# Performance work log

Hardware: AMD Instinct MI355X
Metric: run time of the kernel (lower is better)

The kernel has to match this reference:

```python
import jax, jax.numpy as jnp
import numpy as np

B, LTEXT, LVIS, D, H = 16, 128, 4096, 1024, 16
HD = D // H


def setup_inputs() -> dict:
    key = jax.random.key(0)
    ks = jax.random.split(key, 8)
    s = 0.02
    return {
        'hidden_states': jax.random.normal(ks[0], (B, LVIS, D), jnp.float32),
        'text_states': jax.random.normal(ks[1], (LTEXT, B, D), jnp.float32),
        'Wq': jax.random.normal(ks[2], (D, D), jnp.float32) * s,
        'bq': jnp.zeros((D,), jnp.float32),
        'Wk': jax.random.normal(ks[3], (D, D), jnp.float32) * s,
        'bk': jnp.zeros((D,), jnp.float32),
        'Wv': jax.random.normal(ks[4], (D, D), jnp.float32) * s,
        'bv': jnp.zeros((D,), jnp.float32),
        'Wo': jax.random.normal(ks[5], (D, D), jnp.float32) * s,
        'bo': jnp.zeros((D,), jnp.float32),
    }


def reference(hidden_states, text_states, Wq, bq, Wk, bk, Wv, bv, Wo, bo):
    # text_states: (L_text, B, D) -- code unpacks text_len, bsz from dims 0,1
    # hidden_states: (B, L_vis, D) -- key/value source
    Ltext, bsz, d = text_states.shape
    Lvis = hidden_states.shape[1]
    scale = HD ** -0.5

    # projections (torch Linear x @ W.T + b, here W stored already transposed)
    q = (text_states @ Wq + bq) * scale
    # faithful to torch .view: flatten memory then reshape to (B, Ltext, H, hd)
    q = q.reshape(bsz, Ltext, H, HD).transpose(0, 2, 1, 3)        # (B,H,Lt,hd)
    k = (hidden_states @ Wk + bk).reshape(bsz, Lvis, H, HD).transpose(0, 2, 1, 3)
    v = (hidden_states @ Wv + bv).reshape(bsz, Lvis, H, HD).transpose(0, 2, 1, 3)

    attn = jax.nn.softmax(jnp.einsum('bhtd,bhsd->bhts', q, k), axis=-1)  # (B,H,Lt,Lv)
    text_guided_vision = jnp.einsum('bhts,bhsd->bhtd', attn, v)          # (B,H,Lt,hd)
    # second matmul with transposed attention weights: P^T @ (P V)
    out = jnp.einsum('bhts,bhtd->bhsd', attn, text_guided_vision)        # (B,H,Lv,hd)

    out = out.transpose(0, 2, 1, 3).reshape(bsz, Lvis, d)
    return out @ Wo + bo
```

## Files before the change

### kernel.cpp

```cpp
#include <hip/hip_runtime.h>
#include <stdint.h>

typedef short  s16x8 __attribute__((ext_vector_type(8)));
typedef float  f32x4 __attribute__((ext_vector_type(4)));
typedef unsigned short u16x4 __attribute__((ext_vector_type(4)));

__device__ __forceinline__ unsigned short f2bf(float f) {
  unsigned u = __builtin_bit_cast(unsigned, f);
  u = (u + 0x7fffu + ((u >> 16) & 1u)) >> 16;
  return (unsigned short)u;
}

__device__ __forceinline__ void glds16(const void* g, void* l) {
  __builtin_amdgcn_global_load_lds((const __attribute__((address_space(1))) void*)g,
                                   (__attribute__((address_space(3))) void*)l, 16, 0, 0);
}

__device__ __forceinline__ f32x4 mfma16(s16x8 a, s16x8 b, f32x4 c) {
  return __builtin_amdgcn_mfma_f32_16x16x32_bf16(a, b, c, 0, 0, 0);
}

#define VM4 asm volatile("s_waitcnt vmcnt(4)" ::: "memory")
#define VM0 asm volatile("s_waitcnt vmcnt(0)" ::: "memory")

__global__ __launch_bounds__(256) void kt_cvt(const float* __restrict__ X,
                                              unsigned short* __restrict__ Y) {
  const size_t N8 = (size_t)16 * 4096 * 1024 / 8;
  for (size_t i = (size_t)blockIdx.x * 256 + threadIdx.x; i < N8;
       i += (size_t)gridDim.x * 256) {
    const float* g = X + i * 8;
    f32x4 a = *(const f32x4*)g;
    f32x4 b = *(const f32x4*)(g + 4);
    s16x8 o;
    o[0]=f2bf(a[0]); o[1]=f2bf(a[1]); o[2]=f2bf(a[2]); o[3]=f2bf(a[3]);
    o[4]=f2bf(b[0]); o[5]=f2bf(b[1]); o[6]=f2bf(b[2]); o[7]=f2bf(b[3]);
    *(s16x8*)(Y + i * 8) = o;
  }
}

__global__ void kt_transpose(const float* __restrict__ W, unsigned short* __restrict__ WT) {
  __shared__ float tile[64][65];
  int n0 = blockIdx.x * 64, k0 = blockIdx.y * 64;
  int tx = threadIdx.x, ty = threadIdx.y;
  #pragma unroll
  for (int r = ty; r < 64; r += 4)
    tile[r][tx] = W[(size_t)(k0 + r) * 1024 + n0 + tx];
  __syncthreads();
  #pragma unroll
  for (int r = ty; r < 64; r += 4)
    WT[(size_t)(n0 + r) * 1024 + k0 + tx] = f2bf(tile[tx][r]);
}

__global__ __launch_bounds__(256, 2) void kt_gemm_q(
    const float* __restrict__ Ain, const unsigned short* __restrict__ BT,
    const float* __restrict__ bias, unsigned short* __restrict__ Cout) {
  __shared__ __align__(16) unsigned short As[128 * 32];
  __shared__ __align__(16) unsigned short Bs[128 * 32];
  const int tid = threadIdx.x, lane = tid & 63, wave = tid >> 6;
  const int l15 = lane & 15, quad = lane >> 4;
  const int wr = wave >> 1, wc = wave & 1;
  const int n0 = blockIdx.x * 128, m0 = blockIdx.y * 128;

  f32x4 acc[4][4] = {};
  for (int k0 = 0; k0 < 1024; k0 += 32) {
    __syncthreads();
    #pragma unroll
    for (int i = 0; i < 2; ++i) {
      int rowb = (wave * 2 + i) * 16 + (lane >> 2);
      glds16(BT + (size_t)(n0 + rowb) * 1024 + k0 + (lane & 3) * 8,
             &Bs[(wave * 2 + i) * 512]);
    }
    {
      const float* A = Ain;
      int row = tid >> 1, ks = (tid & 1) * 16;
      const float* g = &A[(size_t)(m0 + row) * 1024 + k0 + ks];
      f32x4 fa = *(const f32x4*)(g);
      f32x4 fb = *(const f32x4*)(g + 4);
      f32x4 fc = *(const f32x4*)(g + 8);
      f32x4 fd = *(const f32x4*)(g + 12);
      s16x8 lo, hi;
      lo[0]=f2bf(fa[0]); lo[1]=f2bf(fa[1]); lo[2]=f2bf(fa[2]); lo[3]=f2bf(fa[3]);
      lo[4]=f2bf(fb[0]); lo[5]=f2bf(fb[1]); lo[6]=f2bf(fb[2]); lo[7]=f2bf(fb[3]);
      hi[0]=f2bf(fc[0]); hi[1]=f2bf(fc[1]); hi[2]=f2bf(fc[2]); hi[3]=f2bf(fc[3]);
      hi[4]=f2bf(fd[0]); hi[5]=f2bf(fd[1]); hi[6]=f2bf(fd[2]); hi[7]=f2bf(fd[3]);
      *(s16x8*)&As[row * 32 + ks] = lo;
      *(s16x8*)&As[row * 32 + ks + 8] = hi;
    }
    __syncthreads();
    s16x8 a[4], b[4];
    #pragma unroll
    for (int i = 0; i < 4; ++i) a[i] = *(const s16x8*)&As[(wr * 64 + i * 16 + l15) * 32 + quad * 8];
    #pragma unroll
    for (int j = 0; j < 4; ++j) b[j] = *(const s16x8*)&Bs[(wc * 64 + j * 16 + l15) * 32 + quad * 8];
    #pragma unroll
    for (int i = 0; i < 4; ++i)
      #pragma unroll
      for (int j = 0; j < 4; ++j) acc[i][j] = mfma16(a[i], b[j], acc[i][j]);
  }
  #pragma unroll
  for (int j = 0; j < 4; ++j) {
    int col = n0 + wc * 64 + j * 16 + l15;
    float bv = bias[col];
    #pragma unroll
    for (int i = 0; i < 4; ++i)
      #pragma unroll
      for (int r = 0; r < 4; ++r) {
        int row = m0 + wr * 64 + i * 16 + quad * 4 + r;
        float v = (acc[i][j][r] + bv) * 0.125f;
        size_t idx = ((size_t)((row >> 7) * 16 + (col >> 6)) * 128 + (row & 127)) * 64 + (col & 63);
        Cout[idx] = f2bf(v);
      }
  }
}

template <int MODE>
__global__ __launch_bounds__(512, 2) void kt_gemm256(
    const unsigned short* __restrict__ A, const unsigned short* __restrict__ BT,
    const float* __restrict__ bias0, const float* __restrict__ bias1,
    void* __restrict__ out0, void* __restrict__ out1) {
  constexpr int NN = (MODE == 0) ? 8 : 4;
  constexpr int CHUNK = (MODE == 0) ? 256 : 128;
  __shared__ __align__(16) unsigned short lds[65536];
  const int tid = threadIdx.x, lane = tid & 63, wave = tid >> 6;
  const int l15 = lane & 15, quad = lane >> 4;
  const int wr = wave >> 2, wc = wave & 3;
  const int r0 = lane >> 3, sck = (lane & 7) ^ r0;
  const int bid = blockIdx.x;
  const int logical = (bid & 7) * CHUNK + (bid >> 3);
  const int nblk = logical & (NN - 1), mblk = logical / NN;
  const int n0 = nblk * 256, m0 = mblk * 256;
  const unsigned short* Asrc = A + (size_t)m0 * 1024;
  const unsigned short* Bsrc = BT + (size_t)n0 * 1024;

  f32x4 acc[8][4] = {};
  s16x8 bf_[4][2];

  auto stageA = [&](int t, int h, int buf) {
    #pragma unroll
    for (int is = 0; is < 2; ++is) {
      int c = wave * 2 + is;
      glds16(Asrc + (size_t)(h * 128 + c * 8 + r0) * 1024 + t * 64 + sck * 8,
             &lds[buf * 32768 + h * 8192 + c * 512]);
    }
  };
  auto stageB = [&](int t, int h, int buf) {
    #pragma unroll
    for (int is = 0; is < 2; ++is) {
      int c = wave * 2 + is;
      glds16(Bsrc + (size_t)(h * 128 + c * 8 + r0) * 1024 + t * 64 + sck * 8,
             &lds[buf * 32768 + 16384 + h * 8192 + c * 512]);
    }
  };

  stageA(0, 0, 0); stageA(0, 1, 0); stageB(0, 0, 0); stageB(0, 1, 0);
  stageB(1, 0, 1); stageB(1, 1, 1);
  VM4;
  __builtin_amdgcn_s_barrier();

  #pragma unroll 1
  for (int it = 0; it < 8; ++it) {
    const bool last = (it == 7);
    const int te = 2 * it;
    #pragma unroll
    for (int half = 0; half < 2; ++half) {
      const int buf = half;
      #pragma unroll
      for (int p = 0; p < 4; ++p) {
        if (p == 0) {
          #pragma unroll
          for (int j = 0; j < 4; ++j)
            #pragma unroll
            for (int kk = 0; kk < 2; ++kk) {
              int r = (wc & 1) * 64 + j * 16 + l15;
              bf_[j][kk] = *(const s16x8*)&lds[buf * 32768 + 16384 + (wc >> 1) * 8192
                                               + r * 64 + (((kk * 4 + quad) ^ (r & 7)) << 3)];
            }
        }
        s16x8 af[2][2];
        #pragma unroll
        for (int ii = 0; ii < 2; ++ii)
          #pragma unroll
          for (int kk = 0; kk < 2; ++kk) {
            int r = (p * 2 + ii) * 16 + l15;
            af[ii][kk] = *(const s16x8*)&lds[buf * 32768 + wr * 8192
                                             + r * 64 + (((kk * 4 + quad) ^ (r & 7)) << 3)];
          }
        if (half == 0) {
          if (p == 0) { stageA(te + 1, 0, 1); stageA(te + 1, 1, 1); }
          else if (p == 1) { if (!last) stageB(te + 2, 0, 0); }
          else if (p == 2) { if (!last) stageB(te + 2, 1, 0); }
        } else {
          if (p == 0) { if (!last) stageA(te + 2, 0, 0); }
          else if (p == 1) { if (!last) { stageA(te + 2, 1, 0); stageB(te + 3, 0, 1); } }
          else if (p == 2) { if (!last) stageB(te + 3, 1, 1); }
        }
        __builtin_amdgcn_s_barrier();
        __builtin_amdgcn_s_setprio(1);
        #pragma unroll
        for (int ii = 0; ii < 2; ++ii)
          #pragma unroll
          for (int j = 0; j < 4; ++j)
            #pragma unroll
            for (int kk = 0; kk < 2; ++kk)
              acc[p * 2 + ii][j] = mfma16(af[ii][kk], bf_[j][kk], acc[p * 2 + ii][j]);
        __builtin_amdgcn_s_setprio(0);
        if (p == 3) {
          if (half == 0) { if (last) { VM0; } else { VM4; } }
          else           { if (!last) { VM4; } }
        }
        __builtin_amdgcn_s_barrier();
      }
    }
  }

  const int bb = m0 >> 12;
  const bool isV = (MODE == 0) && (n0 >= 1024);
  const float* bias = isV ? bias1 : bias0;
  #pragma unroll
  for (int j = 0; j < 4; ++j) {
    const int colg = n0 + wc * 64 + j * 16 + l15;
    const int c1 = colg & 1023;
    const float bv = bias[c1];
    const int hcol = c1 >> 6, dcol = c1 & 63;
    #pragma unroll
    for (int i = 0; i < 8; ++i) {
      const int row0 = m0 + wr * 128 + i * 16 + quad * 4;
      const int s = row0 & 4095;
      if constexpr (MODE == 0) {
        if (isV) {
          size_t base = (((size_t)bb * 16 + hcol) * 64 + dcol) * 4096 + s;
          u16x4 w;
          #pragma unroll
          for (int r = 0; r < 4; ++r) w[r] = f2bf(acc[i][j][r] + bv);
          *(u16x4*)&((unsigned short*)out1)[base] = w;
        } else {
          unsigned short* Ko = (unsigned short*)out0;
          size_t base = (((size_t)bb * 16 + hcol) * 4096 + s) * 64 + dcol;
          #pragma unroll
          for (int r = 0; r < 4; ++r) Ko[base + (size_t)r * 64] = f2bf(acc[i][j][r] + bv);
        }
      } else {
        float* O = (float*)out0;
        size_t base = (size_t)row0 * 1024 + colg;
        #pragma unroll
        for (int r = 0; r < 4; ++r) O[base + (size_t)r * 1024] = acc[i][j][r] + bv;
      }
    }
  }
}

__global__ __launch_bounds__(512, 4) void kt_attn1(
    const unsigned short* __restrict__ Qb, const unsigned short* __restrict__ Kb,
    const unsigned short* __restrict__ Vt, float* __restrict__ RpT,
    float* __restrict__ Zp) {
  __shared__ __align__(16) unsigned short Ks[2][128 * 64];
  __shared__ __align__(16) unsigned short Vts[2][64 * 128];
  __shared__ __align__(16) unsigned short Es[8][16 * 40];
  const int tid = threadIdx.x, lane = tid & 63, wave = tid >> 6;
  const int l15 = lane & 15, quad = lane >> 4;
  const int bid = blockIdx.x;
  const int lid = (bid & 7) * 128 + (bid >> 3);
  const int qidx = lid & 3, bh = lid >> 2;
  const size_t kbase = (size_t)bh * 4096 * 64;
  const size_t vbase = (size_t)bh * 64 * 4096;
  s16x8 qa[2];
  #pragma unroll
  for (int kk = 0; kk < 2; ++kk)
    qa[kk] = *(const s16x8*)&Qb[((size_t)bh * 128 + wave * 16 + l15) * 64 + kk * 32 + quad * 8];
  s16x8 bones;
  { unsigned short o = (l15 == 0) ? (unsigned short)0x3F80 : (unsigned short)0;
    #pragma unroll
    for (int c2 = 0; c2 < 8; ++c2) bones[c2] = (short)o; }
  f32x4 Racc[4] = {};
  f32x4 Zacc = {};

  auto stage = [&](int ch, int buf) {
    const int s0 = qidx * 1024 + ch * 128;
    #pragma unroll
    for (int i = 0; i < 2; ++i) {
      int srow = wave * 16 + i * 8 + (lane >> 3);
      int ck = (lane & 7) ^ (srow & 7);
      glds16(Kb + kbase + (size_t)(s0 + srow) * 64 + ck * 8,
             &Ks[buf][(wave * 16 + i * 8) * 64]);
    }
    #pragma unroll
    for (int i = 0; i < 2; ++i) {
      int drow = wave * 8 + i * 4 + (lane >> 4);
      int ck = (lane & 15) ^ (drow & 15);
      glds16(Vt + vbase + (size_t)drow * 4096 + s0 + ck * 8,
             &Vts[buf][(wave * 8 + i * 4) * 128]);
    }
  };

  stage(0, 0);
  VM0;
  __syncthreads();

  #pragma unroll 1
  for (int ch = 0; ch < 8; ++ch) {
    const int buf = ch & 1;
    if (ch < 7) stage(ch + 1, buf ^ 1);
    f32x4 Sacc[8] = {};
    #pragma unroll
    for (int kk = 0; kk < 2; ++kk)
      #pragma unroll
      for (int jh = 0; jh < 2; ++jh) {
        s16x8 bk[4];
        #pragma unroll
        for (int j = 0; j < 4; ++j) {
          int r = (jh * 4 + j) * 16 + l15;
          bk[j] = *(const s16x8*)&Ks[buf][r * 64 + (((kk * 4 + quad) ^ (r & 7)) << 3)];
        }
        #pragma unroll
        for (int j = 0; j < 4; ++j)
          Sacc[jh * 4 + j] = mfma16(qa[kk], bk[j], Sacc[jh * 4 + j]);
      }
    #pragma unroll
    for (int kk2 = 0; kk2 < 4; ++kk2) {
      #pragma unroll
      for (int jl = 0; jl < 2; ++jl) {
        int j = kk2 * 2 + jl;
        #pragma unroll
        for (int r = 0; r < 4; ++r)
          Es[wave][(quad * 4 + r) * 40 + jl * 16 + l15] = f2bf(__expf(Sacc[j][r]));
      }
      s16x8 ea = *(const s16x8*)&Es[wave][l15 * 40 + quad * 8];
      s16x8 bv[4];
      #pragma unroll
      for (int jd = 0; jd < 4; ++jd) {
        int r = jd * 16 + l15;
        bv[jd] = *(const s16x8*)&Vts[buf][r * 128 + (((kk2 * 4 + quad) ^ (r & 15)) << 3)];
      }
      #pragma unroll
      for (int jd = 0; jd < 4; ++jd) Racc[jd] = mfma16(ea, bv[jd], Racc[jd]);
      Zacc = mfma16(ea, bones, Zacc);
    }
    if (ch < 7) VM0;
    __syncthreads();
  }
  int t0 = wave * 16 + quad * 4;
  #pragma unroll
  for (int jd = 0; jd < 4; ++jd) {
    int d = jd * 16 + l15;
    *(f32x4*)&RpT[(((size_t)qidx * 256 + bh) * 64 + d) * 128 + t0] = Racc[jd];
  }
  if (l15 == 0) {
    #pragma unroll
    for (int r = 0; r < 4; ++r)
      Zp[((size_t)qidx * 256 + bh) * 128 + t0 + r] = Zacc[r];
  }
}

__global__ void kt_reduce(const float* __restrict__ RpT, const float* __restrict__ Zp,
                          unsigned short* __restrict__ Gt) {
  size_t id = (size_t)blockIdx.x * 256 + threadIdx.x;
  int t = (int)(id & 127);
  size_t bh = id >> 13;
  float z = 0.f, r = 0.f;
  #pragma unroll
  for (int q = 0; q < 4; ++q) {
    z += Zp[(size_t)q * 32768 + bh * 128 + t];
    r += RpT[(size_t)q * 2097152 + id];
  }
  Gt[id] = f2bf(r / (z * z));
}

__global__ __launch_bounds__(256, 2) void kt_attn2(
    const unsigned short* __restrict__ Qb, const unsigned short* __restrict__ Kb,
    const unsigned short* __restrict__ Gt, unsigned short* __restrict__ Ao) {
  __shared__ __align__(16) unsigned short Ks[2][64 * 64];
  __shared__ __align__(16) unsigned short EsT[64 * 136];
  const int tid = threadIdx.x, lane = tid & 63, wave = tid >> 6;
  const int l15 = lane & 15, quad = lane >> 4;
  const int bid = blockIdx.x;
  const int lid = (bid & 7) * 128 + (bid >> 3);
  const int c = lid & 3, bh = lid >> 2;
  const int h = bh & 15, b = bh >> 4;
  s16x8 qf[8][2], gf[4][4];
  #pragma unroll
  for (int jt = 0; jt < 8; ++jt)
    #pragma unroll
    for (int kk = 0; kk < 2; ++kk)
      qf[jt][kk] = *(const s16x8*)&Qb[((size_t)bh * 128 + jt * 16 + l15) * 64 + kk * 32 + quad * 8];
  #pragma unroll
  for (int jd = 0; jd < 4; ++jd)
    #pragma unroll
    for (int kk = 0; kk < 4; ++kk)
      gf[jd][kk] = *(const s16x8*)&Gt[((size_t)bh * 64 + jd * 16 + l15) * 128 + kk * 32 + quad * 8];
  const size_t kbase = (size_t)bh * 4096 * 64;

  auto stage = [&](int it, int buf) {
    const int s0 = c * 1024 + it * 64;
    #pragma unroll
    for (int i = 0; i < 2; ++i) {
      int srow = wave * 16 + i * 8 + (lane >> 3);
      int ck = (lane & 7) ^ (srow & 7);
      glds16(Kb + kbase + (size_t)(s0 + srow) * 64 + ck * 8,
             &Ks[buf][(wave * 16 + i * 8) * 64]);
    }
  };

  stage(0, 0);
  VM0;
  __syncthreads();

  #pragma unroll 1
  for (int it = 0; it < 16; ++it) {
    const int buf = it & 1;
    if (it < 15) stage(it + 1, buf ^ 1);
    const int s0 = c * 1024 + it * 64;
    f32x4 Sacc[8] = {};
    #pragma unroll
    for (int kk = 0; kk < 2; ++kk) {
      int r = wave * 16 + l15;
      s16x8 a = *(const s16x8*)&Ks[buf][r * 64 + (((kk * 4 + quad) ^ (r & 7)) << 3)];
      #pragma unroll
      for (int jt = 0; jt < 8; ++jt) Sacc[jt] = mfma16(a, qf[jt][kk], Sacc[jt]);
    }
    #pragma unroll
    for (int jt = 0; jt < 8; ++jt)
      #pragma unroll
      for (int r = 0; r < 4; ++r)
        EsT[(wave * 16 + quad * 4 + r) * 136 + jt * 16 + l15] = f2bf(__expf(Sacc[jt][r]));
    f32x4 Oacc[4] = {};
    #pragma unroll
    for (int kk = 0; kk < 4; ++kk) {
      s16x8 ea = *(const s16x8*)&EsT[(wave * 16 + l15) * 136 + kk * 32 + quad * 8];
      #pragma unroll
      for (int jd = 0; jd < 4; ++jd) Oacc[jd] = mfma16(ea, gf[jd][kk], Oacc[jd]);
    }
    #pragma unroll
    for (int jd = 0; jd < 4; ++jd)
      #pragma unroll
      for (int r = 0; r < 4; ++r) {
        int s = s0 + wave * 16 + quad * 4 + r;
        int d = jd * 16 + l15;
        Ao[((size_t)b * 4096 + s) * 1024 + h * 64 + d] = f2bf(Oacc[jd][r]);
      }
    if (it < 15) VM0;
    __syncthreads();
  }
}

extern "C" void kernel_launch(void* const* d_in, const int* in_sizes, int n_in,
                              void* d_out, int out_size, void* d_ws, size_t ws_size,
                              hipStream_t stream) {
  const float* hidden = (const float*)d_in[0];
  const float* text   = (const float*)d_in[1];
  const float* Wq = (const float*)d_in[2]; const float* bq = (const float*)d_in[3];
  const float* Wk = (const float*)d_in[4]; const float* bk = (const float*)d_in[5];
  const float* Wv = (const float*)d_in[6]; const float* bv = (const float*)d_in[7];
  const float* Wo = (const float*)d_in[8]; const float* bo = (const float*)d_in[9];
  char* ws = (char*)d_ws;
  unsigned short* WqT = (unsigned short*)(ws + (size_t)0);
  unsigned short* WkT = (unsigned short*)(ws + ((size_t)2 << 20));
  unsigned short* WvT = (unsigned short*)(ws + ((size_t)4 << 20));
  unsigned short* WoT = (unsigned short*)(ws + ((size_t)6 << 20));
  unsigned short* Qb  = (unsigned short*)(ws + ((size_t)8 << 20));
  unsigned short* Kb  = (unsigned short*)(ws + ((size_t)12 << 20));
  unsigned short* Vt  = (unsigned short*)(ws + ((size_t)140 << 20));
  unsigned short* Hb  = (unsigned short*)(ws + ((size_t)268 << 20));
  unsigned short* Ao  = (unsigned short*)(ws + ((size_t)268 << 20));
  float*          RpT = (float*)(ws + ((size_t)396 << 20));
  float*          Zp  = (float*)(ws + ((size_t)428 << 20));
  unsigned short* Gt  = (unsigned short*)(ws + ((size_t)429 << 20));

  dim3 blk(256);
  kt_transpose<<<dim3(16, 16), dim3(64, 4), 0, stream>>>(Wq, WqT);
  kt_transpose<<<dim3(16, 16), dim3(64, 4), 0, stream>>>(Wk, WkT);
  kt_transpose<<<dim3(16, 16), dim3(64, 4), 0, stream>>>(Wv, WvT);
  kt_transpose<<<dim3(16, 16), dim3(64, 4), 0, stream>>>(Wo, WoT);
  kt_cvt<<<dim3(2048), blk, 0, stream>>>(hidden, Hb);
  kt_gemm_q<<<dim3(8, 16), blk, 0, stream>>>(text, WqT, bq, Qb);
  kt_gemm256<0><<<dim3(2048), dim3(512), 0, stream>>>(Hb, WkT, bk, bv, Kb, Vt);
  kt_attn1<<<dim3(1024), dim3(512), 0, stream>>>(Qb, Kb, Vt, RpT, Zp);
  kt_reduce<<<dim3(8192), blk, 0, stream>>>(RpT, Zp, Gt);
  kt_attn2<<<dim3(1024), blk, 0, stream>>>(Qb, Kb, Gt, Ao);
  kt_gemm256<2><<<dim3(1024), dim3(512), 0, stream>>>(Ao, WoT, bo, nullptr, d_out, nullptr);
}
```

Before: 1.161 ms.

## Restructure GEMM mainloop to 4-stage K=32 pipeline with new swizzle

Replaces the double-buffered K=64 tile mainloop of the 256x256 bf16 GEMM with a four-buffer ring of K=32 tiles, prefetching three tiles ahead. The LDS swizzle changes to match the 32-element rows. Each step splits the MFMA work into two halves, with A and B staging interleaved between them. The aim is to hide global-load latency better and simplify the schedule. The cost is twice as many barriers per K, and the smaller K slices mean fewer MFMAs between each sync.

```diff
diff --git a/kernel.cpp b/kernel.cpp
--- a/kernel.cpp
+++ b/kernel.cpp
@@ -20,6 +20,7 @@
   return __builtin_amdgcn_mfma_f32_16x16x32_bf16(a, b, c, 0, 0, 0);
 }
 
+#define VM8 asm volatile("s_waitcnt vmcnt(8)" ::: "memory")
 #define VM4 asm volatile("s_waitcnt vmcnt(4)" ::: "memory")
 #define VM0 asm volatile("s_waitcnt vmcnt(0)" ::: "memory")
 
@@ -124,7 +125,8 @@
   const int tid = threadIdx.x, lane = tid & 63, wave = tid >> 6;
   const int l15 = lane & 15, quad = lane >> 4;
   const int wr = wave >> 2, wc = wave & 3;
-  const int r0 = lane >> 3, sck = (lane & 7) ^ r0;
+  const int swl = (l15 ^ (l15 >> 2)) & 3;
+  const int ckS = ((lane & 3) ^ ((lane >> 2) & 3) ^ ((lane >> 4) & 3));
   const int bid = blockIdx.x;
   const int logical = (bid & 7) * CHUNK + (bid >> 3);
   const int nblk = logical & (NN - 1), mblk = logical / NN;
@@ -133,85 +135,79 @@
   const unsigned short* Bsrc = BT + (size_t)n0 * 1024;
 
   f32x4 acc[8][4] = {};
-  s16x8 bf_[4][2];
-
-  auto stageA = [&](int t, int h, int buf) {
-    #pragma unroll
-    for (int is = 0; is < 2; ++is) {
-      int c = wave * 2 + is;
-      glds16(Asrc + (size_t)(h * 128 + c * 8 + r0) * 1024 + t * 64 + sck * 8,
-             &lds[buf * 32768 + h * 8192 + c * 512]);
+
+  auto stageA = [&](int t, int buf) {
+    #pragma unroll
+    for (int h = 0; h < 2; ++h) {
+      int row = h * 128 + wave * 16 + (lane >> 2);
+      glds16(Asrc + (size_t)row * 1024 + t * 32 + ckS * 8,
+             &lds[buf * 8192 + (h * 128 + wave * 16) * 32]);
     }
   };
-  auto stageB = [&](int t, int h, int buf) {
-    #pragma unroll
-    for (int is = 0; is < 2; ++is) {
-      int c = wave * 2 + is;
-      glds16(Bsrc + (size_t)(h * 128 + c * 8 + r0) * 1024 + t * 64 + sck * 8,
-             &lds[buf * 32768 + 16384 + h * 8192 + c * 512]);
+  auto stageB = [&](int t, int buf) {
+    #pragma unroll
+    for (int h = 0; h < 2; ++h) {
+      int row = h * 128 + wave * 16 + (lane >> 2);
+      glds16(Bsrc + (size_t)row * 1024 + t * 32 + ckS * 8,
+             &lds[32768 + buf * 8192 + (h * 128 + wave * 16) * 32]);
     }
   };
 
-  stageA(0, 0, 0); stageA(0, 1, 0); stageB(0, 0, 0); stageB(0, 1, 0);
-  stageB(1, 0, 1); stageB(1, 1, 1);
-  VM4;
+  auto tile_step = [&](int t, int buf, int pbuf, bool do_stage, int vm) {
+    s16x8 bfr[4], af[4];
+    #pragma unroll
+    for (int j = 0; j < 4; ++j) {
+      int r = wc * 64 + j * 16 + l15;
+      bfr[j] = *(const s16x8*)&lds[32768 + buf * 8192 + r * 32 + ((quad ^ swl) << 3)];
+    }
+    #pragma unroll
+    for (int ii = 0; ii < 4; ++ii) {
+      int r = wr * 128 + ii * 16 + l15;
+      af[ii] = *(const s16x8*)&lds[buf * 8192 + r * 32 + ((quad ^ swl) << 3)];
+    }
+    if (do_stage) stageA(t + 3, pbuf);
+    __builtin_amdgcn_s_barrier();
+    __builtin_amdgcn_s_setprio(1);
+    #pragma unroll
+    for (int ii = 0; ii < 4; ++ii)
+      #pragma unroll
+      for (int j = 0; j < 4; ++j)
+        acc[ii][j] = mfma16(af[ii], bfr[j], acc[ii][j]);
+    __builtin_amdgcn_s_setprio(0);
+    __builtin_amdgcn_s_barrier();
+    #pragma unroll
+    for (int ii = 0; ii < 4; ++ii) {
+      int r = wr * 128 + (4 + ii) * 16 + l15;
+      af[ii] = *(const s16x8*)&lds[buf * 8192 + r * 32 + ((quad ^ swl) << 3)];
+    }
+    if (do_stage) stageB(t + 3, pbuf);
+    __builtin_amdgcn_s_barrier();
+    __builtin_amdgcn_s_setprio(1);
+    #pragma unroll
+    for (int ii = 0; ii < 4; ++ii)
+      #pragma unroll
+      for (int j = 0; j < 4; ++j)
+        acc[4 + ii][j] = mfma16(af[ii], bfr[j], acc[4 + ii][j]);
+    __builtin_amdgcn_s_setprio(0);
+    if (vm == 8) { VM8; } else if (vm == 4) { VM4; } else if (vm == 0) { VM0; }
+    __builtin_amdgcn_s_barrier();
+  };
+
+  stageA(0, 0); stageB(0, 0); stageA(1, 1); stageB(1, 1); stageA(2, 2); stageB(2, 2);
+  VM8;
   __builtin_amdgcn_s_barrier();
 
   #pragma unroll 1
-  for (int it = 0; it < 8; ++it) {
-    const bool last = (it == 7);
-    const int te = 2 * it;
-    #pragma unroll
-    for (int half = 0; half < 2; ++half) {
-      const int buf = half;
-      #pragma unroll
-      for (int p = 0; p < 4; ++p) {
-        if (p == 0) {
-          #pragma unroll
-          for (int j = 0; j < 4; ++j)
-            #pragma unroll
-            for (int kk = 0; kk < 2; ++kk) {
-              int r = (wc & 1) * 64 + j * 16 + l15;
-              bf_[j][kk] = *(const s16x8*)&lds[buf * 32768 + 16384 + (wc >> 1) * 8192
-                                               + r * 64 + (((kk * 4 + quad) ^ (r & 7)) << 3)];
-            }
-        }
-        s16x8 af[2][2];
-        #pragma unroll
-        for (int ii = 0; ii < 2; ++ii)
-          #pragma unroll
-          for (int kk = 0; kk < 2; ++kk) {
-            int r = (p * 2 + ii) * 16 + l15;
-            af[ii][kk] = *(const s16x8*)&lds[buf * 32768 + wr * 8192
-                                             + r * 64 + (((kk * 4 + quad) ^ (r & 7)) << 3)];
-          }
-        if (half == 0) {
-          if (p == 0) { stageA(te + 1, 0, 1); stageA(te + 1, 1, 1); }
-          else if (p == 1) { if (!last) stageB(te + 2, 0, 0); }
-          else if (p == 2) { if (!last) stageB(te + 2, 1, 0); }
-        } else {
-          if (p == 0) { if (!last) stageA(te + 2, 0, 0); }
-          else if (p == 1) { if (!last) { stageA(te + 2, 1, 0); stageB(te + 3, 0, 1); } }
-          else if (p == 2) { if (!last) stageB(te + 3, 1, 1); }
-        }
-        __builtin_amdgcn_s_barrier();
-        __builtin_amdgcn_s_setprio(1);
-        #pragma unroll
-        for (int ii = 0; ii < 2; ++ii)
-          #pragma unroll
-          for (int j = 0; j < 4; ++j)
-            #pragma unroll
-            for (int kk = 0; kk < 2; ++kk)
-              acc[p * 2 + ii][j] = mfma16(af[ii][kk], bf_[j][kk], acc[p * 2 + ii][j]);
-        __builtin_amdgcn_s_setprio(0);
-        if (p == 3) {
-          if (half == 0) { if (last) { VM0; } else { VM4; } }
-          else           { if (!last) { VM4; } }
-        }
-        __builtin_amdgcn_s_barrier();
-      }
-    }
-  }
+  for (int ot = 0; ot < 7; ++ot) {
+    tile_step(ot * 4 + 0, 0, 3, true, 8);
+    tile_step(ot * 4 + 1, 1, 0, true, 8);
+    tile_step(ot * 4 + 2, 2, 1, true, 8);
+    tile_step(ot * 4 + 3, 3, 2, true, 8);
+  }
+  tile_step(28, 0, 3, true, 8);
+  tile_step(29, 1, 0, false, 4);
+  tile_step(30, 2, 1, false, 0);
+  tile_step(31, 3, 2, false, -1);
 
   const int bb = m0 >> 12;
   const bool isV = (MODE == 0) && (n0 >= 1024);
```

Result: no change. 1.165 ms (+0.4%).

## Deepen attention K/V prefetch to four-buffer ring with three stages in flight

Applied to the files above, without the earlier changes.

Both attention kernels switch from a double-buffered LDS staging loop to a four-slot ring that keeps three tiles in flight. Each iteration now waits with a partial vmcnt and does one barrier instead of draining all loads. attn1 also halves its chunk to 64 keys, doubling the iteration count while keeping LDS size the same. The goal is to hide global-to-LDS latency behind MFMA work. In attn2, the global stores inside the loop also count against vmcnt, so the partial wait may end up draining the prefetch loads as well.

```diff
diff --git a/kernel.cpp b/kernel.cpp
--- a/kernel.cpp
+++ b/kernel.cpp
@@ -21,6 +21,7 @@
 }
 
 #define VM4 asm volatile("s_waitcnt vmcnt(4)" ::: "memory")
+#define VM2 asm volatile("s_waitcnt vmcnt(2)" ::: "memory")
 #define VM0 asm volatile("s_waitcnt vmcnt(0)" ::: "memory")
 
 __global__ __launch_bounds__(256) void kt_cvt(const float* __restrict__ X,
@@ -253,8 +254,8 @@
     const unsigned short* __restrict__ Qb, const unsigned short* __restrict__ Kb,
     const unsigned short* __restrict__ Vt, float* __restrict__ RpT,
     float* __restrict__ Zp) {
-  __shared__ __align__(16) unsigned short Ks[2][128 * 64];
-  __shared__ __align__(16) unsigned short Vts[2][64 * 128];
+  __shared__ __align__(16) unsigned short Ks[4][64 * 64];
+  __shared__ __align__(16) unsigned short Vts[4][64 * 64];
   __shared__ __align__(16) unsigned short Es[8][16 * 40];
   const int tid = threadIdx.x, lane = tid & 63, wave = tid >> 6;
   const int l15 = lane & 15, quad = lane >> 4;
@@ -275,48 +276,36 @@
   f32x4 Zacc = {};
 
   auto stage = [&](int ch, int buf) {
-    const int s0 = qidx * 1024 + ch * 128;
-    #pragma unroll
-    for (int i = 0; i < 2; ++i) {
-      int srow = wave * 16 + i * 8 + (lane >> 3);
-      int ck = (lane & 7) ^ (srow & 7);
-      glds16(Kb + kbase + (size_t)(s0 + srow) * 64 + ck * 8,
-             &Ks[buf][(wave * 16 + i * 8) * 64]);
-    }
-    #pragma unroll
-    for (int i = 0; i < 2; ++i) {
-      int drow = wave * 8 + i * 4 + (lane >> 4);
-      int ck = (lane & 15) ^ (drow & 15);
-      glds16(Vt + vbase + (size_t)drow * 4096 + s0 + ck * 8,
-             &Vts[buf][(wave * 8 + i * 4) * 128]);
-    }
+    const int s0 = qidx * 1024 + ch * 64;
+    const int rr = lane >> 3, ck = (lane & 7) ^ rr;
+    glds16(Kb + kbase + (size_t)(s0 + wave * 8 + rr) * 64 + ck * 8,
+           &Ks[buf][wave * 8 * 64]);
+    glds16(Vt + vbase + (size_t)(wave * 8 + rr) * 4096 + s0 + ck * 8,
+           &Vts[buf][wave * 8 * 64]);
   };
 
-  stage(0, 0);
-  VM0;
-  __syncthreads();
+  stage(0, 0); stage(1, 1); stage(2, 2);
 
   #pragma unroll 1
-  for (int ch = 0; ch < 8; ++ch) {
-    const int buf = ch & 1;
-    if (ch < 7) stage(ch + 1, buf ^ 1);
-    f32x4 Sacc[8] = {};
-    #pragma unroll
-    for (int kk = 0; kk < 2; ++kk)
-      #pragma unroll
-      for (int jh = 0; jh < 2; ++jh) {
-        s16x8 bk[4];
-        #pragma unroll
-        for (int j = 0; j < 4; ++j) {
-          int r = (jh * 4 + j) * 16 + l15;
-          bk[j] = *(const s16x8*)&Ks[buf][r * 64 + (((kk * 4 + quad) ^ (r & 7)) << 3)];
-        }
-        #pragma unroll
-        for (int j = 0; j < 4; ++j)
-          Sacc[jh * 4 + j] = mfma16(qa[kk], bk[j], Sacc[jh * 4 + j]);
-      }
-    #pragma unroll
-    for (int kk2 = 0; kk2 < 4; ++kk2) {
+  for (int ch = 0; ch < 16; ++ch) {
+    const int buf = ch & 3;
+    if (ch <= 13) { VM4; } else if (ch == 14) { VM2; } else { VM0; }
+    __syncthreads();
+    if (ch < 13) stage(ch + 3, (ch + 3) & 3);
+    f32x4 Sacc[4] = {};
+    #pragma unroll
+    for (int kk = 0; kk < 2; ++kk) {
+      s16x8 bk[4];
+      #pragma unroll
+      for (int j = 0; j < 4; ++j) {
+        int r = j * 16 + l15;
+        bk[j] = *(const s16x8*)&Ks[buf][r * 64 + (((kk * 4 + quad) ^ (r & 7)) << 3)];
+      }
+      #pragma unroll
+      for (int j = 0; j < 4; ++j) Sacc[j] = mfma16(qa[kk], bk[j], Sacc[j]);
+    }
+    #pragma unroll
+    for (int kk2 = 0; kk2 < 2; ++kk2) {
       #pragma unroll
       for (int jl = 0; jl < 2; ++jl) {
         int j = kk2 * 2 + jl;
@@ -329,14 +318,12 @@
       #pragma unroll
       for (int jd = 0; jd < 4; ++jd) {
         int r = jd * 16 + l15;
-        bv[jd] = *(const s16x8*)&Vts[buf][r * 128 + (((kk2 * 4 + quad) ^ (r & 15)) << 3)];
+        bv[jd] = *(const s16x8*)&Vts[buf][r * 64 + (((kk2 * 4 + quad) ^ (r & 7)) << 3)];
       }
       #pragma unroll
       for (int jd = 0; jd < 4; ++jd) Racc[jd] = mfma16(ea, bv[jd], Racc[jd]);
       Zacc = mfma16(ea, bones, Zacc);
     }
-    if (ch < 7) VM0;
-    __syncthreads();
   }
   int t0 = wave * 16 + quad * 4;
   #pragma unroll
@@ -368,7 +355,7 @@
 __global__ __launch_bounds__(256, 2) void kt_attn2(
     const unsigned short* __restrict__ Qb, const unsigned short* __restrict__ Kb,
     const unsigned short* __restrict__ Gt, unsigned short* __restrict__ Ao) {
-  __shared__ __align__(16) unsigned short Ks[2][64 * 64];
+  __shared__ __align__(16) unsigned short Ks[4][64 * 64];
   __shared__ __align__(16) unsigned short EsT[64 * 136];
   const int tid = threadIdx.x, lane = tid & 63, wave = tid >> 6;
   const int l15 = lane & 15, quad = lane >> 4;
@@ -400,14 +387,14 @@
     }
   };
 
-  stage(0, 0);
-  VM0;
-  __syncthreads();
+  stage(0, 0); stage(1, 1); stage(2, 2);
 
   #pragma unroll 1
   for (int it = 0; it < 16; ++it) {
-    const int buf = it & 1;
-    if (it < 15) stage(it + 1, buf ^ 1);
+    const int buf = it & 3;
+    if (it <= 13) { VM4; } else if (it == 14) { VM2; } else { VM0; }
+    __syncthreads();
+    if (it < 13) stage(it + 3, (it + 3) & 3);
     const int s0 = c * 1024 + it * 64;
     f32x4 Sacc[8] = {};
     #pragma unroll
@@ -437,8 +424,6 @@
         int d = jd * 16 + l15;
         Ao[((size_t)b * 4096 + s) * 1024 + h * 64 + d] = f2bf(Oacc[jd][r]);
       }
-    if (it < 15) VM0;
-    __syncthreads();
   }
 }
 
```

After: 1.161 ms. No clear change (+0.0%).

## Load K/V fragments directly from global memory in attention kernels, drop LDS staging

Applied to the files above, without the earlier changes.

Both attention kernels stop staging K (and transposed V) tiles in shared memory through async global-to-LDS copies with double buffering. Each wave now reads its MFMA operand fragments straight from global memory, and the block-wide barriers and vmcnt waits are removed. The per-wave exp scratch buffers are double-buffered so that no barrier is needed between iterations. This cuts LDS traffic and synchronization, and in kt_attn1 raises possible occupancy, but it gives up cross-wave reuse of the K/V tiles and the prefetch that hid global load latency.

```diff
diff --git a/kernel.cpp b/kernel.cpp
--- a/kernel.cpp
+++ b/kernel.cpp
@@ -253,9 +253,7 @@
     const unsigned short* __restrict__ Qb, const unsigned short* __restrict__ Kb,
     const unsigned short* __restrict__ Vt, float* __restrict__ RpT,
     float* __restrict__ Zp) {
-  __shared__ __align__(16) unsigned short Ks[2][128 * 64];
-  __shared__ __align__(16) unsigned short Vts[2][64 * 128];
-  __shared__ __align__(16) unsigned short Es[8][16 * 40];
+  __shared__ __align__(16) unsigned short Es[8][2][16 * 40];
   const int tid = threadIdx.x, lane = tid & 63, wave = tid >> 6;
   const int l15 = lane & 15, quad = lane >> 4;
   const int bid = blockIdx.x;
@@ -274,32 +272,9 @@
   f32x4 Racc[4] = {};
   f32x4 Zacc = {};
 
-  auto stage = [&](int ch, int buf) {
-    const int s0 = qidx * 1024 + ch * 128;
-    #pragma unroll
-    for (int i = 0; i < 2; ++i) {
-      int srow = wave * 16 + i * 8 + (lane >> 3);
-      int ck = (lane & 7) ^ (srow & 7);
-      glds16(Kb + kbase + (size_t)(s0 + srow) * 64 + ck * 8,
-             &Ks[buf][(wave * 16 + i * 8) * 64]);
-    }
-    #pragma unroll
-    for (int i = 0; i < 2; ++i) {
-      int drow = wave * 8 + i * 4 + (lane >> 4);
-      int ck = (lane & 15) ^ (drow & 15);
-      glds16(Vt + vbase + (size_t)drow * 4096 + s0 + ck * 8,
-             &Vts[buf][(wave * 8 + i * 4) * 128]);
-    }
-  };
-
-  stage(0, 0);
-  VM0;
-  __syncthreads();
-
   #pragma unroll 1
   for (int ch = 0; ch < 8; ++ch) {
-    const int buf = ch & 1;
-    if (ch < 7) stage(ch + 1, buf ^ 1);
+    const int s0 = qidx * 1024 + ch * 128;
     f32x4 Sacc[8] = {};
     #pragma unroll
     for (int kk = 0; kk < 2; ++kk)
@@ -307,36 +282,33 @@
       for (int jh = 0; jh < 2; ++jh) {
         s16x8 bk[4];
         #pragma unroll
-        for (int j = 0; j < 4; ++j) {
-          int r = (jh * 4 + j) * 16 + l15;
-          bk[j] = *(const s16x8*)&Ks[buf][r * 64 + (((kk * 4 + quad) ^ (r & 7)) << 3)];
-        }
+        for (int j = 0; j < 4; ++j)
+          bk[j] = *(const s16x8*)&Kb[kbase + (size_t)(s0 + (jh * 4 + j) * 16 + l15) * 64
+                                     + kk * 32 + quad * 8];
         #pragma unroll
         for (int j = 0; j < 4; ++j)
           Sacc[jh * 4 + j] = mfma16(qa[kk], bk[j], Sacc[jh * 4 + j]);
       }
     #pragma unroll
     for (int kk2 = 0; kk2 < 4; ++kk2) {
+      unsigned short* es = &Es[wave][kk2 & 1][0];
       #pragma unroll
       for (int jl = 0; jl < 2; ++jl) {
         int j = kk2 * 2 + jl;
         #pragma unroll
         for (int r = 0; r < 4; ++r)
-          Es[wave][(quad * 4 + r) * 40 + jl * 16 + l15] = f2bf(__expf(Sacc[j][r]));
-      }
-      s16x8 ea = *(const s16x8*)&Es[wave][l15 * 40 + quad * 8];
+          es[(quad * 4 + r) * 40 + jl * 16 + l15] = f2bf(__expf(Sacc[j][r]));
+      }
+      s16x8 ea = *(const s16x8*)&es[l15 * 40 + quad * 8];
       s16x8 bv[4];
       #pragma unroll
-      for (int jd = 0; jd < 4; ++jd) {
-        int r = jd * 16 + l15;
-        bv[jd] = *(const s16x8*)&Vts[buf][r * 128 + (((kk2 * 4 + quad) ^ (r & 15)) << 3)];
-      }
+      for (int jd = 0; jd < 4; ++jd)
+        bv[jd] = *(const s16x8*)&Vt[vbase + (size_t)(jd * 16 + l15) * 4096
+                                    + s0 + kk2 * 32 + quad * 8];
       #pragma unroll
       for (int jd = 0; jd < 4; ++jd) Racc[jd] = mfma16(ea, bv[jd], Racc[jd]);
       Zacc = mfma16(ea, bones, Zacc);
     }
-    if (ch < 7) VM0;
-    __syncthreads();
   }
   int t0 = wave * 16 + quad * 4;
   #pragma unroll
@@ -365,11 +337,10 @@
   Gt[id] = f2bf(r / (z * z));
 }
 
-__global__ __launch_bounds__(256, 2) void kt_attn2(
+__global__ __launch_bounds__(256) void kt_attn2(
     const unsigned short* __restrict__ Qb, const unsigned short* __restrict__ Kb,
     const unsigned short* __restrict__ Gt, unsigned short* __restrict__ Ao) {
-  __shared__ __align__(16) unsigned short Ks[2][64 * 64];
-  __shared__ __align__(16) unsigned short EsT[64 * 136];
+  __shared__ __align__(16) unsigned short EsT[2][64 * 136];
   const int tid = threadIdx.x, lane = tid & 63, wave = tid >> 6;
   const int l15 = lane & 15, quad = lane >> 4;
   const int bid = blockIdx.x;
@@ -389,43 +360,27 @@
       gf[jd][kk] = *(const s16x8*)&Gt[((size_t)bh * 64 + jd * 16 + l15) * 128 + kk * 32 + quad * 8];
   const size_t kbase = (size_t)bh * 4096 * 64;
 
-  auto stage = [&](int it, int buf) {
-    const int s0 = c * 1024 + it * 64;
-    #pragma unroll
-    for (int i = 0; i < 2; ++i) {
-      int srow = wave * 16 + i * 8 + (lane >> 3);
-      int ck = (lane & 7) ^ (srow & 7);
-      glds16(Kb + kbase + (size_t)(s0 + srow) * 64 + ck * 8,
-             &Ks[buf][(wave * 16 + i * 8) * 64]);
-    }
-  };
-
-  stage(0, 0);
-  VM0;
-  __syncthreads();
-
   #pragma unroll 1
   for (int it = 0; it < 16; ++it) {
-    const int buf = it & 1;
-    if (it < 15) stage(it + 1, buf ^ 1);
     const int s0 = c * 1024 + it * 64;
     f32x4 Sacc[8] = {};
     #pragma unroll
     for (int kk = 0; kk < 2; ++kk) {
-      int r = wave * 16 + l15;
-      s16x8 a = *(const s16x8*)&Ks[buf][r * 64 + (((kk * 4 + quad) ^ (r & 7)) << 3)];
+      s16x8 a = *(const s16x8*)&Kb[kbase + (size_t)(s0 + wave * 16 + l15) * 64
+                                   + kk * 32 + quad * 8];
       #pragma unroll
       for (int jt = 0; jt < 8; ++jt) Sacc[jt] = mfma16(a, qf[jt][kk], Sacc[jt]);
     }
+    unsigned short* est = &EsT[it & 1][0];
     #pragma unroll
     for (int jt = 0; jt < 8; ++jt)
       #pragma unroll
       for (int r = 0; r < 4; ++r)
-        EsT[(wave * 16 + quad * 4 + r) * 136 + jt * 16 + l15] = f2bf(__expf(Sacc[jt][r]));
+        est[(wave * 16 + quad * 4 + r) * 136 + jt * 16 + l15] = f2bf(__expf(Sacc[jt][r]));
     f32x4 Oacc[4] = {};
     #pragma unroll
     for (int kk = 0; kk < 4; ++kk) {
-      s16x8 ea = *(const s16x8*)&EsT[(wave * 16 + l15) * 136 + kk * 32 + quad * 8];
+      s16x8 ea = *(const s16x8*)&est[(wave * 16 + l15) * 136 + kk * 32 + quad * 8];
       #pragma unroll
       for (int jd = 0; jd < 4; ++jd) Oacc[jd] = mfma16(ea, gf[jd][kk], Oacc[jd]);
     }
@@ -437,8 +392,6 @@
         int d = jd * 16 + l15;
         Ao[((size_t)b * 4096 + s) * 1024 + h * 64 + d] = f2bf(Oacc[jd][r]);
       }
-    if (it < 15) VM0;
-    __syncthreads();
   }
 }
 
```

Result: slower. 1.320 ms (+13.8%).
